# Kernel optimization log

Hardware: AMD Instinct MI355X
Metric: run time of the kernel (lower is better)

Reference implementation:

```python
import jax, jax.numpy as jnp
import numpy as np

N, C, H, W = 8, 512, 56, 56
CI = 256  # inter_channels = in_channels // reduction


def setup_inputs() -> dict:
    key = jax.random.key(0)
    ks = jax.random.split(key, 9)
    std = 0.01
    return {
        "x": jax.random.normal(ks[0], (N, C, H, W), dtype=jnp.float32),
        "W_g": jax.random.normal(ks[1], (CI, C), dtype=jnp.float32) * std,
        "b_g": jnp.zeros((CI,), dtype=jnp.float32),
        "W_theta": jax.random.normal(ks[2], (CI, C), dtype=jnp.float32) * std,
        "b_theta": jnp.zeros((CI,), dtype=jnp.float32),
        "W_phi": jax.random.normal(ks[3], (CI, C), dtype=jnp.float32) * std,
        "b_phi": jnp.zeros((CI,), dtype=jnp.float32),
        "W_out": jax.random.normal(ks[4], (C, CI), dtype=jnp.float32) * std,
        "b_out": jax.random.normal(ks[5], (C,), dtype=jnp.float32) * std,
    }


def _proj(Wt, b, xf):
    # 1x1 conv == channel GEMM over flattened spatial positions: (n, o, L)
    return jnp.einsum('oc,ncl->nol', Wt, xf) + b[None, :, None]


def reference(x, W_g, b_g, W_theta, b_theta, W_phi, b_phi, W_out, b_out):
    n, c, h, w = x.shape
    L = h * w
    xf = x.reshape(n, c, L)

    g_x = _proj(W_g, b_g, xf).transpose(0, 2, 1)          # (n, L, ci)
    theta_x = _proj(W_theta, b_theta, xf).transpose(0, 2, 1)  # (n, L, ci)
    phi_x = _proj(W_phi, b_phi, xf)                        # (n, ci, L)

    ci = theta_x.shape[-1]
    # embedded_gaussian with use_scale=True
    pairwise = jnp.einsum('nqc,nck->nqk', theta_x, phi_x) / jnp.sqrt(
        jnp.asarray(ci, dtype=x.dtype))
    pairwise = jax.nn.softmax(pairwise, axis=-1)           # (n, L, L)

    y = jnp.einsum('nqk,nkc->nqc', pairwise, g_x)          # (n, L, ci)
    y = y.transpose(0, 2, 1)                               # (n, ci, L)
    out = _proj(W_out, b_out, y).reshape(n, c, h, w)
    return x + out
```

## Files before the change

### kernel.cpp

```cpp
#include <hip/hip_runtime.h>
#include <stdint.h>

#define NB 8
#define CC 512
#define LL 3136
#define CIN 256

typedef __attribute__((ext_vector_type(8))) short bf8;
typedef __attribute__((ext_vector_type(4))) float f4;

__device__ __forceinline__ f4 mfma_bf16(bf8 a, bf8 b, f4 c) {
  return __builtin_amdgcn_mfma_f32_16x16x32_bf16(a, b, c, 0, 0, 0);
}

__device__ __forceinline__ unsigned short f2bf(float f) {
  unsigned int u = __float_as_uint(f);
  u += 0x7FFFu + ((u >> 16) & 1u);
  return (unsigned short)(u >> 16);
}

__device__ __forceinline__ void gload_lds16(const unsigned short* g, unsigned short* l) {
  __builtin_amdgcn_global_load_lds(
      (const __attribute__((address_space(1))) void*)g,
      (__attribute__((address_space(3))) void*)l, 16, 0, 0);
}

__global__ void k_convw(const float* Wth, const float* Wph, const float* Wg, const float* Wout,
                        unsigned short* dst) {
  int i = blockIdx.x * 256 + threadIdx.x;
  int which = i >> 17;
  int off = i & 131071;
  const float* s = which == 0 ? Wth : which == 1 ? Wph : which == 2 ? Wg : Wout;
  dst[i] = f2bf(s[off]);
}

__global__ __launch_bounds__(256) void k_xT(const float* x, unsigned short* xT) {
  __shared__ unsigned short tile[64][66];
  const int lt = blockIdx.x, n = blockIdx.y, ct = blockIdx.z;
  const int t = threadIdx.x;
  const float* xb = x + (size_t)n * CC * LL + (size_t)(ct * 64) * LL + lt * 64;
  const int tl = t & 63, trow = t >> 6;
#pragma unroll
  for (int i = 0; i < 16; ++i) {
    int c = i * 4 + trow;
    tile[c][tl] = f2bf(xb[(size_t)c * LL + tl]);
  }
  __syncthreads();
  unsigned short* xo = xT + (size_t)n * LL * CC + (size_t)(lt * 64) * CC + ct * 64;
  const int tc = t & 63, lrow = t >> 6;
#pragma unroll
  for (int i = 0; i < 16; ++i) {
    int l = i * 4 + lrow;
    xo[(size_t)l * CC + tc] = tile[tc][l];
  }
}

__global__ __launch_bounds__(256, 3) void k_proj(const unsigned short* Wbf,
    const float* bth, const float* bph, const float* bg,
    const unsigned short* xT, unsigned short* QT, unsigned short* KT, unsigned short* Vb) {
  __shared__ unsigned short wtile[2][8192];
  __shared__ unsigned short xtile[2][4096];
  const int bid = blockIdx.x;
  const int n = bid & 7, t = bid >> 3;
  const int lt = t % 49, z = t / 49;
  const int proj = z >> 1, cith = z & 1;
  const int tid = threadIdx.x;
  const int wave = tid >> 6, lane = tid & 63;
  const int quad = lane >> 4, c16 = lane & 15;

  const unsigned short* Wg = Wbf + proj * 131072 + (size_t)(cith * 128) * CC;
  const unsigned short* Xg = xT + (size_t)n * LL * CC + (size_t)(lt * 64) * CC;

  auto issue = [&](int chunk, int b) {
    const int cb = chunk * 64;
#pragma unroll
    for (int i = 0; i < 4; ++i) {
      int seg = i * 4 + wave;
      int p = seg * 64 + lane;
      int r = p >> 3, sl = p & 7, g = sl ^ (r & 7);
      gload_lds16(Wg + (size_t)r * CC + cb + g * 8, &wtile[b][seg * 512]);
    }
#pragma unroll
    for (int i = 0; i < 2; ++i) {
      int seg = i * 4 + wave;
      int p = seg * 64 + lane;
      int r = p >> 3, sl = p & 7, g = sl ^ (r & 7);
      gload_lds16(Xg + (size_t)r * CC + cb + g * 8, &xtile[b][seg * 512]);
    }
  };

  const f4 zz = {0.f, 0.f, 0.f, 0.f};
  f4 acc[2][4];
#pragma unroll
  for (int i = 0; i < 2; ++i)
#pragma unroll
    for (int j = 0; j < 4; ++j) acc[i][j] = zz;

  issue(0, 0);
  for (int chunk = 0; chunk < 8; ++chunk) {
    __syncthreads();
    if (chunk + 1 < 8) issue(chunk + 1, (chunk + 1) & 1);
    const int bb = chunk & 1;
#pragma unroll
    for (int kc = 0; kc < 2; ++kc) {
      const int slot = (kc * 4 + quad) ^ (c16 & 7);
      bf8 wf[2], xf[4];
#pragma unroll
      for (int sub = 0; sub < 2; ++sub)
        wf[sub] = *(const bf8*)(&wtile[bb][(wave * 32 + sub * 16 + c16) * 64 + slot * 8]);
#pragma unroll
      for (int nt = 0; nt < 4; ++nt)
        xf[nt] = *(const bf8*)(&xtile[bb][(nt * 16 + c16) * 64 + slot * 8]);
      if (proj < 2) {
#pragma unroll
        for (int sub = 0; sub < 2; ++sub)
#pragma unroll
          for (int nt = 0; nt < 4; ++nt)
            acc[sub][nt] = mfma_bf16(wf[sub], xf[nt], acc[sub][nt]);
      } else {
#pragma unroll
        for (int sub = 0; sub < 2; ++sub)
#pragma unroll
          for (int nt = 0; nt < 4; ++nt)
            acc[sub][nt] = mfma_bf16(xf[nt], wf[sub], acc[sub][nt]);
      }
    }
  }

  if (proj < 2) {
    const float* bias = proj == 0 ? bth : bph;
    unsigned short* dst = proj == 0 ? QT : KT;
#pragma unroll
    for (int sub = 0; sub < 2; ++sub) {
      const int ciB = cith * 128 + wave * 32 + sub * 16 + quad * 4;
      const float b0 = bias[ciB + 0], b1 = bias[ciB + 1];
      const float b2 = bias[ciB + 2], b3 = bias[ciB + 3];
#pragma unroll
      for (int nt = 0; nt < 4; ++nt) {
        int l = lt * 64 + nt * 16 + c16;
        ushort4 v;
        v.x = f2bf(acc[sub][nt][0] + b0);
        v.y = f2bf(acc[sub][nt][1] + b1);
        v.z = f2bf(acc[sub][nt][2] + b2);
        v.w = f2bf(acc[sub][nt][3] + b3);
        *(ushort4*)(dst + ((size_t)n * LL + l) * CIN + ciB) = v;
      }
    }
  } else {
#pragma unroll
    for (int sub = 0; sub < 2; ++sub) {
      const int ci = cith * 128 + wave * 32 + sub * 16 + c16;
      const float bv = bg[ci];
#pragma unroll
      for (int nt = 0; nt < 4; ++nt) {
        int l = lt * 64 + nt * 16 + quad * 4;
        ushort4 v;
        v.x = f2bf(acc[sub][nt][0] + bv);
        v.y = f2bf(acc[sub][nt][1] + bv);
        v.z = f2bf(acc[sub][nt][2] + bv);
        v.w = f2bf(acc[sub][nt][3] + bv);
        *(ushort4*)(Vb + ((size_t)n * CIN + ci) * LL + l) = v;
      }
    }
  }
}

__global__ __launch_bounds__(256, 2) void k_attn(const unsigned short* QT, const unsigned short* KT,
                                                 const unsigned short* Vb, unsigned short* O) {
  __shared__ unsigned short kbuf[2][8192];
  __shared__ unsigned short vbuf[2][8192];
  __shared__ __align__(16) unsigned short plds[4][16][40];
  const int bid = blockIdx.x;
  const int n = bid & 7, qt = bid >> 3;
  const int tid = threadIdx.x;
  const int wave = tid >> 6, lane = tid & 63;
  const int quad = lane >> 4, c16 = lane & 15;
  const int q0 = qt * 64 + wave * 16;
  const unsigned short* Qb = QT + ((size_t)n * LL + q0) * CIN;
  const unsigned short* Kbase = KT + (size_t)n * LL * CIN;
  const unsigned short* Vbase = Vb + (size_t)n * CIN * LL;

  const float qs = 0.09016844005556021f;
  bf8 qf[8];
#pragma unroll
  for (int kc = 0; kc < 8; ++kc) {
    bf8 q = *(const bf8*)(Qb + (size_t)c16 * CIN + kc * 32 + quad * 8);
#pragma unroll
    for (int e = 0; e < 8; ++e) {
      float f = __uint_as_float(((unsigned)(unsigned short)q[e]) << 16) * qs;
      q[e] = (short)f2bf(f);
    }
    qf[kc] = q;
  }

  const f4 zz = {0.f, 0.f, 0.f, 0.f};
  f4 o[16];
#pragma unroll
  for (int i = 0; i < 16; ++i) o[i] = zz;
  float s[4] = {0.f, 0.f, 0.f, 0.f};
  const int vslot = quad ^ ((c16 >> 1) & 3);

  auto issue = [&](int kt, int b) {
    const int k0 = kt * 32;
    const unsigned short* Kg = Kbase + (size_t)k0 * CIN;
    const unsigned short* Vg = Vbase + k0;
#pragma unroll
    for (int i = 0; i < 4; ++i) {
      int seg = i * 4 + wave;
      int idx = seg * 64 + lane;
      {
        int r = idx >> 5, sl = idx & 31, g = sl ^ r;
        gload_lds16(Kg + r * CIN + g * 8, &kbuf[b][seg * 512]);
      }
      {
        int r = idx >> 2, sl = idx & 3, g = sl ^ ((r >> 1) & 3);
        gload_lds16(Vg + (size_t)r * LL + g * 8, &vbuf[b][seg * 512]);
      }
    }
  };

  issue(0, 0);
  for (int kt = 0; kt < 98; ++kt) {
    __syncthreads();
    if (kt + 1 < 98) issue(kt + 1, (kt + 1) & 1);
    const int b = kt & 1;
    const unsigned short* kb = &kbuf[b][0];
    const unsigned short* vbp = &vbuf[b][0];

    f4 sc0 = zz, sc1 = zz;
#pragma unroll
    for (int kc = 0; kc < 8; ++kc) {
      int sl0 = (kc * 4 + quad) ^ c16;
      bf8 b0 = *(const bf8*)(kb + c16 * 256 + sl0 * 8);
      bf8 b1 = *(const bf8*)(kb + (16 + c16) * 256 + (sl0 ^ 16) * 8);
      sc0 = mfma_bf16(qf[kc], b0, sc0);
      sc1 = mfma_bf16(qf[kc], b1, sc1);
    }
#pragma unroll
    for (int r = 0; r < 4; ++r) {
      float p0 = __builtin_amdgcn_exp2f(sc0[r]);
      float p1 = __builtin_amdgcn_exp2f(sc1[r]);
      s[r] += p0 + p1;
      plds[wave][quad * 4 + r][c16] = f2bf(p0);
      plds[wave][quad * 4 + r][16 + c16] = f2bf(p1);
    }
    bf8 a = *(const bf8*)(&plds[wave][c16][quad * 8]);
#pragma unroll
    for (int cg = 0; cg < 16; ++cg) {
      bf8 bv = *(const bf8*)(vbp + cg * 512 + c16 * 32 + vslot * 8);
      o[cg] = mfma_bf16(a, bv, o[cg]);
    }
  }

#pragma unroll
  for (int r = 0; r < 4; ++r) {
#pragma unroll
    for (int off = 1; off < 16; off <<= 1) s[r] += __shfl_xor(s[r], off);
  }
  float inv[4];
#pragma unroll
  for (int r = 0; r < 4; ++r) inv[r] = 1.f / s[r];

  unsigned short* Ob = O + ((size_t)n * LL + q0) * CIN;
#pragma unroll
  for (int cg = 0; cg < 16; ++cg)
#pragma unroll
    for (int r = 0; r < 4; ++r)
      Ob[(size_t)(quad * 4 + r) * CIN + cg * 16 + c16] = f2bf(o[cg][r] * inv[r]);
}

__global__ __launch_bounds__(256, 3) void k_out(const unsigned short* O, const unsigned short* Wo,
    const float* bout, const float* x, float* out) {
  __shared__ unsigned short wtile[2][8192];
  __shared__ unsigned short otile[2][4096];
  const int bid = blockIdx.x;
  const int n = bid & 7, t = bid >> 3;
  const int lt = t % 49, cth = t / 49;
  const int tid = threadIdx.x;
  const int wave = tid >> 6, lane = tid & 63;
  const int quad = lane >> 4, c16 = lane & 15;

  const unsigned short* Wg = Wo + (size_t)(cth * 128) * CIN;
  const unsigned short* Og = O + ((size_t)n * LL + lt * 64) * CIN;

  auto issue = [&](int chunk, int b) {
    const int cb = chunk * 64;
#pragma unroll
    for (int i = 0; i < 4; ++i) {
      int seg = i * 4 + wave;
      int p = seg * 64 + lane;
      int r = p >> 3, sl = p & 7, g = sl ^ (r & 7);
      gload_lds16(Wg + (size_t)r * CIN + cb + g * 8, &wtile[b][seg * 512]);
    }
#pragma unroll
    for (int i = 0; i < 2; ++i) {
      int seg = i * 4 + wave;
      int p = seg * 64 + lane;
      int r = p >> 3, sl = p & 7, g = sl ^ (r & 7);
      gload_lds16(Og + (size_t)r * CIN + cb + g * 8, &otile[b][seg * 512]);
    }
  };

  const f4 zz = {0.f, 0.f, 0.f, 0.f};
  f4 acc[4][2];
#pragma unroll
  for (int i = 0; i < 4; ++i)
#pragma unroll
    for (int j = 0; j < 2; ++j) acc[i][j] = zz;

  issue(0, 0);
  for (int chunk = 0; chunk < 4; ++chunk) {
    __syncthreads();
    if (chunk + 1 < 4) issue(chunk + 1, (chunk + 1) & 1);
    const int bb = chunk & 1;
#pragma unroll
    for (int kc = 0; kc < 2; ++kc) {
      const int slot = (kc * 4 + quad) ^ (c16 & 7);
      bf8 wf[2], ofr[4];
#pragma unroll
      for (int sub = 0; sub < 2; ++sub)
        wf[sub] = *(const bf8*)(&wtile[bb][(wave * 32 + sub * 16 + c16) * 64 + slot * 8]);
#pragma unroll
      for (int nt = 0; nt < 4; ++nt)
        ofr[nt] = *(const bf8*)(&otile[bb][(nt * 16 + c16) * 64 + slot * 8]);
#pragma unroll
      for (int nt = 0; nt < 4; ++nt)
#pragma unroll
        for (int sub = 0; sub < 2; ++sub)
          acc[nt][sub] = mfma_bf16(ofr[nt], wf[sub], acc[nt][sub]);
    }
  }

#pragma unroll
  for (int sub = 0; sub < 2; ++sub) {
    const int c = cth * 128 + wave * 32 + sub * 16 + c16;
    const float bv = bout[c];
#pragma unroll
    for (int nt = 0; nt < 4; ++nt) {
      int l = lt * 64 + nt * 16 + quad * 4;
      size_t base = ((size_t)n * CC + c) * LL + l;
      f4 xv = *(const f4*)(x + base);
      f4 r;
      r[0] = xv[0] + bv + acc[nt][sub][0];
      r[1] = xv[1] + bv + acc[nt][sub][1];
      r[2] = xv[2] + bv + acc[nt][sub][2];
      r[3] = xv[3] + bv + acc[nt][sub][3];
      *(f4*)(out + base) = r;
    }
  }
}

extern "C" void kernel_launch(void* const* d_in, const int* in_sizes, int n_in,
                              void* d_out, int out_size, void* d_ws, size_t ws_size,
                              hipStream_t stream) {
  const float* x     = (const float*)d_in[0];
  const float* W_g   = (const float*)d_in[1];
  const float* b_g   = (const float*)d_in[2];
  const float* W_th  = (const float*)d_in[3];
  const float* b_th  = (const float*)d_in[4];
  const float* W_ph  = (const float*)d_in[5];
  const float* b_ph  = (const float*)d_in[6];
  const float* W_out = (const float*)d_in[7];
  const float* b_out = (const float*)d_in[8];

  char* ws = (char*)d_ws;
  const size_t SZ_W  = 1048576;
  const size_t SZ_P  = 12845056;
  unsigned short* Wbf = (unsigned short*)(ws);
  unsigned short* QT  = (unsigned short*)(ws + SZ_W);
  unsigned short* KT  = (unsigned short*)(ws + SZ_W + SZ_P);
  unsigned short* Vb  = (unsigned short*)(ws + SZ_W + 2 * SZ_P);
  unsigned short* xT  = (unsigned short*)(ws + SZ_W + 3 * SZ_P);
  unsigned short* O   = xT;
  float* out = (float*)d_out;

  k_convw<<<2048, 256, 0, stream>>>(W_th, W_ph, W_g, W_out, Wbf);
  k_xT<<<dim3(49, 8, 8), 256, 0, stream>>>(x, xT);
  k_proj<<<2352, 256, 0, stream>>>(Wbf, b_th, b_ph, b_g, xT, QT, KT, Vb);
  k_attn<<<392, 256, 0, stream>>>(QT, KT, Vb, O);
  k_out<<<1568, 256, 0, stream>>>(O, Wbf + 3 * 131072, b_out, x, out);
}
```

Measured before the change: 328.1 us.

## Switch attention kernel to 32x32x16 MFMA with 32 queries per wave

Rewrites the attention kernel to use 32x32x16 bf16 MFMA tiles, giving each wave 32 queries and each block 128 queries. K and V tiles in LDS are reused across twice as many queries, and the MFMA count per tile drops. The softmax denominator is now summed from the bf16-rounded probabilities, and the last partial tile is clamped and its store masked. The grid shrinks to 200 blocks, which lowers parallelism and may leave many compute units idle.

```diff
diff --git a/kernel.cpp b/kernel.cpp
--- a/kernel.cpp
+++ b/kernel.cpp
@@ -8,9 +8,14 @@
 
 typedef __attribute__((ext_vector_type(8))) short bf8;
 typedef __attribute__((ext_vector_type(4))) float f4;
+typedef __attribute__((ext_vector_type(16))) float f16v;
 
 __device__ __forceinline__ f4 mfma_bf16(bf8 a, bf8 b, f4 c) {
   return __builtin_amdgcn_mfma_f32_16x16x32_bf16(a, b, c, 0, 0, 0);
+}
+
+__device__ __forceinline__ f16v mfma32(bf8 a, bf8 b, f16v c) {
+  return __builtin_amdgcn_mfma_f32_32x32x16_bf16(a, b, c, 0, 0, 0);
 }
 
 __device__ __forceinline__ unsigned short f2bf(float f) {
@@ -169,22 +174,24 @@
                                                  const unsigned short* Vb, unsigned short* O) {
   __shared__ unsigned short kbuf[2][8192];
   __shared__ unsigned short vbuf[2][8192];
-  __shared__ __align__(16) unsigned short plds[4][16][40];
+  __shared__ __align__(16) unsigned short plds[4][1280];
   const int bid = blockIdx.x;
-  const int n = bid & 7, qt = bid >> 3;
+  const int n = bid & 7, qb = bid >> 3;
   const int tid = threadIdx.x;
   const int wave = tid >> 6, lane = tid & 63;
-  const int quad = lane >> 4, c16 = lane & 15;
-  const int q0 = qt * 64 + wave * 16;
+  const int l31 = lane & 31, half = lane >> 5;
+  int q0 = qb * 128 + wave * 32;
+  const bool do_store = q0 < LL;
+  if (q0 > LL - 32) q0 = LL - 32;
   const unsigned short* Qb = QT + ((size_t)n * LL + q0) * CIN;
   const unsigned short* Kbase = KT + (size_t)n * LL * CIN;
   const unsigned short* Vbase = Vb + (size_t)n * CIN * LL;
 
   const float qs = 0.09016844005556021f;
-  bf8 qf[8];
-#pragma unroll
-  for (int kc = 0; kc < 8; ++kc) {
-    bf8 q = *(const bf8*)(Qb + (size_t)c16 * CIN + kc * 32 + quad * 8);
+  bf8 qf[16];
+#pragma unroll
+  for (int kc = 0; kc < 16; ++kc) {
+    bf8 q = *(const bf8*)(Qb + (size_t)l31 * CIN + kc * 16 + half * 8);
 #pragma unroll
     for (int e = 0; e < 8; ++e) {
       float f = __uint_as_float(((unsigned)(unsigned short)q[e]) << 16) * qs;
@@ -193,12 +200,12 @@
     qf[kc] = q;
   }
 
-  const f4 zz = {0.f, 0.f, 0.f, 0.f};
-  f4 o[16];
-#pragma unroll
-  for (int i = 0; i < 16; ++i) o[i] = zz;
-  float s[4] = {0.f, 0.f, 0.f, 0.f};
-  const int vslot = quad ^ ((c16 >> 1) & 3);
+  f16v o[8];
+#pragma unroll
+  for (int t = 0; t < 8; ++t)
+#pragma unroll
+    for (int r = 0; r < 16; ++r) o[t][r] = 0.f;
+  float sden = 0.f;
 
   auto issue = [&](int kt, int b) {
     const int k0 = kt * 32;
@@ -219,6 +226,7 @@
     }
   };
 
+  unsigned short* pw = &plds[wave][0];
   issue(0, 0);
   for (int kt = 0; kt < 98; ++kt) {
     __syncthreads();
@@ -227,46 +235,59 @@
     const unsigned short* kb = &kbuf[b][0];
     const unsigned short* vbp = &vbuf[b][0];
 
-    f4 sc0 = zz, sc1 = zz;
-#pragma unroll
-    for (int kc = 0; kc < 8; ++kc) {
-      int sl0 = (kc * 4 + quad) ^ c16;
-      bf8 b0 = *(const bf8*)(kb + c16 * 256 + sl0 * 8);
-      bf8 b1 = *(const bf8*)(kb + (16 + c16) * 256 + (sl0 ^ 16) * 8);
-      sc0 = mfma_bf16(qf[kc], b0, sc0);
-      sc1 = mfma_bf16(qf[kc], b1, sc1);
-    }
-#pragma unroll
-    for (int r = 0; r < 4; ++r) {
-      float p0 = __builtin_amdgcn_exp2f(sc0[r]);
-      float p1 = __builtin_amdgcn_exp2f(sc1[r]);
-      s[r] += p0 + p1;
-      plds[wave][quad * 4 + r][c16] = f2bf(p0);
-      plds[wave][quad * 4 + r][16 + c16] = f2bf(p1);
-    }
-    bf8 a = *(const bf8*)(&plds[wave][c16][quad * 8]);
-#pragma unroll
-    for (int cg = 0; cg < 16; ++cg) {
-      bf8 bv = *(const bf8*)(vbp + cg * 512 + c16 * 32 + vslot * 8);
-      o[cg] = mfma_bf16(a, bv, o[cg]);
-    }
-  }
-
-#pragma unroll
-  for (int r = 0; r < 4; ++r) {
-#pragma unroll
-    for (int off = 1; off < 16; off <<= 1) s[r] += __shfl_xor(s[r], off);
-  }
-  float inv[4];
-#pragma unroll
-  for (int r = 0; r < 4; ++r) inv[r] = 1.f / s[r];
-
-  unsigned short* Ob = O + ((size_t)n * LL + q0) * CIN;
-#pragma unroll
-  for (int cg = 0; cg < 16; ++cg)
-#pragma unroll
-    for (int r = 0; r < 4; ++r)
-      Ob[(size_t)(quad * 4 + r) * CIN + cg * 16 + c16] = f2bf(o[cg][r] * inv[r]);
+    f16v sc;
+#pragma unroll
+    for (int r = 0; r < 16; ++r) sc[r] = 0.f;
+#pragma unroll
+    for (int kc = 0; kc < 16; ++kc) {
+      int slot = (kc * 2 + half) ^ l31;
+      bf8 bfr = *(const bf8*)(kb + l31 * 256 + slot * 8);
+      sc = mfma32(qf[kc], bfr, sc);
+    }
+#pragma unroll
+    for (int r = 0; r < 16; ++r) {
+      float p = __builtin_amdgcn_exp2f(sc[r]);
+      int row = (r & 3) + 8 * (r >> 2) + 4 * half;
+      pw[row * 40 + l31] = f2bf(p);
+    }
+    bf8 af[2];
+#pragma unroll
+    for (int kc2 = 0; kc2 < 2; ++kc2) {
+      af[kc2] = *(const bf8*)(pw + l31 * 40 + kc2 * 16 + half * 8);
+#pragma unroll
+      for (int e = 0; e < 8; ++e)
+        sden += __uint_as_float(((unsigned)(unsigned short)af[kc2][e]) << 16);
+    }
+#pragma unroll
+    for (int t = 0; t < 8; ++t) {
+#pragma unroll
+      for (int kc2 = 0; kc2 < 2; ++kc2) {
+        int slot = (kc2 * 2 + half) ^ ((l31 >> 1) & 3);
+        bf8 v = *(const bf8*)(vbp + (t * 32 + l31) * 32 + slot * 8);
+        o[t] = mfma32(af[kc2], v, o[t]);
+      }
+    }
+  }
+
+  sden += __shfl_xor(sden, 32);
+  sden = 1.f / sden;
+  float inv[16];
+#pragma unroll
+  for (int r = 0; r < 16; ++r) {
+    int row = (r & 3) + 8 * (r >> 2) + 4 * half;
+    inv[r] = __shfl(sden, row);
+  }
+
+  if (do_store) {
+    unsigned short* Ob = O + ((size_t)n * LL + q0) * CIN;
+#pragma unroll
+    for (int t = 0; t < 8; ++t)
+#pragma unroll
+      for (int r = 0; r < 16; ++r) {
+        int row = (r & 3) + 8 * (r >> 2) + 4 * half;
+        Ob[(size_t)row * CIN + t * 32 + l31] = f2bf(o[t][r] * inv[r]);
+      }
+  }
 }
 
 __global__ __launch_bounds__(256, 3) void k_out(const unsigned short* O, const unsigned short* Wo,
@@ -377,6 +398,6 @@
   k_convw<<<2048, 256, 0, stream>>>(W_th, W_ph, W_g, W_out, Wbf);
   k_xT<<<dim3(49, 8, 8), 256, 0, stream>>>(x, xT);
   k_proj<<<2352, 256, 0, stream>>>(Wbf, b_th, b_ph, b_g, xT, QT, KT, Vb);
-  k_attn<<<392, 256, 0, stream>>>(QT, KT, Vb, O);
+  k_attn<<<200, 256, 0, stream>>>(QT, KT, Vb, O);
   k_out<<<1568, 256, 0, stream>>>(O, Wbf + 3 * 131072, b_out, x, out);
 }
```

New measurement: 382.6 us. 16.6% more time.
